# Kernel tuning notes

Hardware: AMD Instinct MI355X
Metric: run time of the kernel (lower is better)

Reference implementation:

```python
import jax, jax.numpy as jnp
import numpy as np

B, S, H, I = 4, 2048, 2048, 8192
LN_EPS = 1e-6  # DeepSpeed inference layer-norm epsilon


def setup_inputs() -> dict:
    key = jax.random.key(0)
    ks = jax.random.split(key, 10)
    return {
        "input": jax.random.normal(ks[0], (B, S, H), dtype=jnp.float32),
        "residual": jax.random.normal(ks[1], (B, S, H), dtype=jnp.float32),
        "residual_norm": jax.random.normal(ks[2], (B, S, H), dtype=jnp.float32),
        "bias": jax.random.normal(ks[3], (H,), dtype=jnp.float32) * 0.02,
        "gamma": jnp.ones((H,), dtype=jnp.float32) + jax.random.normal(ks[4], (H,), dtype=jnp.float32) * 0.02,
        "beta": jax.random.normal(ks[5], (H,), dtype=jnp.float32) * 0.02,
        "inter_w": jax.random.normal(ks[6], (H, I), dtype=jnp.float32) * 0.02,
        "inter_b": jax.random.normal(ks[7], (I,), dtype=jnp.float32) * 0.02,
        "output_w": jax.random.normal(ks[8], (I, H), dtype=jnp.float32) * 0.02,
        "output_b": jax.random.normal(ks[9], (H,), dtype=jnp.float32) * 0.02,
    }


def reference(input, residual, residual_norm, bias, gamma, beta,
              inter_w, inter_b, output_w, output_b):
    # --- mlp_gemm_func (pre-LN path, attn_nw is not None) ---
    # Fused: residual_add = attention_output + attention_bias + residual
    residual_add = input + residual + bias                    # [B,S,H]
    # LayerNorm over hidden dim
    mu = jnp.mean(residual_add, axis=-1, keepdims=True)
    var = jnp.mean(jnp.square(residual_add - mu), axis=-1, keepdims=True)
    ln = (residual_add - mu) * jax.lax.rsqrt(var + LN_EPS) * gamma + beta
    # GEMM + bias + GeLU, then second GEMM
    h = jax.nn.gelu(jnp.einsum("bsh,hi->bsi", ln, inter_w) + inter_b,
                    approximate=False)                        # [B,S,I]
    out = jnp.einsum("bsi,ih->bsh", h, output_w)              # [B,S,H]
    # --- residual_add_func (pre-LN, mlp_after_attn): mlp_out + residual_add + final_bias ---
    return out + residual_add + output_b
```

## Files before the change

kernel.cpp:

```cpp
#include <hip/hip_runtime.h>

typedef __attribute__((ext_vector_type(8))) __bf16 bf16x8;
typedef __attribute__((ext_vector_type(4))) float f32x4;

#define AS1(p) ((const __attribute__((address_space(1))) void*)(uintptr_t)(p))
#define AS3(p) ((__attribute__((address_space(3))) void*)(uint32_t)(uintptr_t)(p))
#define GLD16(gp, lp) __builtin_amdgcn_global_load_lds(AS1(gp), AS3(lp), 16, 0, 0)

static constexpr int Bb = 4, Ss = 2048, Hh = 2048, Ih = 8192;
static constexpr int Mm = Bb * Ss;

__device__ __forceinline__ float gelu_exact(float x) {
    return 0.5f * x * (1.0f + erff(x * 0.70710678118654752440f));
}

__global__ __launch_bounds__(256) void transpose_cvt(const float* __restrict__ src,
                                                     __bf16* __restrict__ dst,
                                                     int R, int C) {
    __shared__ float tile[32][33];
    const int tx = threadIdx.x, ty = threadIdx.y;
    const int cB = blockIdx.x * 32, rB = blockIdx.y * 32;
#pragma unroll
    for (int i = 0; i < 4; ++i)
        tile[ty + i * 8][tx] = src[(size_t)(rB + ty + i * 8) * C + cB + tx];
    __syncthreads();
#pragma unroll
    for (int i = 0; i < 4; ++i)
        dst[(size_t)(cB + ty + i * 8) * R + rB + tx] = (__bf16)tile[tx][ty + i * 8];
}

__global__ __launch_bounds__(256) void fused_ln(const float* __restrict__ input,
                                                const float* __restrict__ residual,
                                                const float* __restrict__ bias,
                                                const float* __restrict__ gamma,
                                                const float* __restrict__ beta,
                                                __bf16* __restrict__ lnb,
                                                __bf16* __restrict__ rab) {
    const int row = blockIdx.x;
    const int tid = threadIdx.x;
    const size_t base = (size_t)row * Hh;
    const int e = tid * 8;

    float4 x0 = *(const float4*)(input + base + e);
    float4 x1 = *(const float4*)(input + base + e + 4);
    float4 r0 = *(const float4*)(residual + base + e);
    float4 r1 = *(const float4*)(residual + base + e + 4);
    float4 b0 = *(const float4*)(bias + e);
    float4 b1 = *(const float4*)(bias + e + 4);

    float s[8];
    s[0] = x0.x + r0.x + b0.x; s[1] = x0.y + r0.y + b0.y;
    s[2] = x0.z + r0.z + b0.z; s[3] = x0.w + r0.w + b0.w;
    s[4] = x1.x + r1.x + b1.x; s[5] = x1.y + r1.y + b1.y;
    s[6] = x1.z + r1.z + b1.z; s[7] = x1.w + r1.w + b1.w;

    float sum = 0.f, sq = 0.f;
#pragma unroll
    for (int j = 0; j < 8; ++j) { sum += s[j]; sq += s[j] * s[j]; }
#pragma unroll
    for (int o = 32; o > 0; o >>= 1) {
        sum += __shfl_xor(sum, o);
        sq  += __shfl_xor(sq, o);
    }
    __shared__ float red[8];
    const int wv = tid >> 6, ln_ = tid & 63;
    if (ln_ == 0) { red[wv] = sum; red[4 + wv] = sq; }
    __syncthreads();
    sum = red[0] + red[1] + red[2] + red[3];
    sq  = red[4] + red[5] + red[6] + red[7];

    const float mu   = sum * (1.0f / Hh);
    const float var  = sq * (1.0f / Hh) - mu * mu;
    const float rstd = rsqrtf(var + 1e-6f);

    float4 g0 = *(const float4*)(gamma + e);
    float4 g1 = *(const float4*)(gamma + e + 4);
    float4 t0 = *(const float4*)(beta + e);
    float4 t1 = *(const float4*)(beta + e + 4);
    float g[8] = {g0.x, g0.y, g0.z, g0.w, g1.x, g1.y, g1.z, g1.w};
    float t[8] = {t0.x, t0.y, t0.z, t0.w, t1.x, t1.y, t1.z, t1.w};

    bf16x8 lv, rv;
#pragma unroll
    for (int j = 0; j < 8; ++j) {
        rv[j] = (__bf16)s[j];
        lv[j] = (__bf16)((s[j] - mu) * rstd * g[j] + t[j]);
    }
    *(bf16x8*)(lnb + base + e) = lv;
    *(bf16x8*)(rab + base + e) = rv;
}

#define CFENCE asm volatile("" ::: "memory")
#define BARX   do { CFENCE; __builtin_amdgcn_s_barrier(); CFENCE; } while (0)
#define SP1 __builtin_amdgcn_s_setprio(1)
#define SP0 __builtin_amdgcn_s_setprio(0)
#define VM2 asm volatile("s_waitcnt vmcnt(2)" ::: "memory")
#define VM0 asm volatile("s_waitcnt vmcnt(0)" ::: "memory")

__device__ __forceinline__ void rdA(bf16x8 (&af)[4][2], const char* p0, const char* p1,
                                    const int off) {
#pragma unroll
    for (int m = 0; m < 4; ++m) {
        af[m][0] = *(const bf16x8*)(p0 + off + m * 2048);
        af[m][1] = *(const bf16x8*)(p1 + off + m * 2048);
    }
}
__device__ __forceinline__ void rdB(bf16x8 (&bf)[2][2], const char* p0, const char* p1,
                                    const int off) {
#pragma unroll
    for (int n = 0; n < 2; ++n) {
        bf[n][0] = *(const bf16x8*)(p0 + off + n * 2048);
        bf[n][1] = *(const bf16x8*)(p1 + off + n * 2048);
    }
}
template <int MH, int NH>
__device__ __forceinline__ void mfmaQ(const bf16x8 (&a)[4][2], const bf16x8 (&b)[2][2],
                                      f32x4 (&acc)[8][4]) {
#pragma unroll
    for (int ks = 0; ks < 2; ++ks)
#pragma unroll
        for (int m = 0; m < 4; ++m)
#pragma unroll
            for (int n = 0; n < 2; ++n)
                acc[MH * 4 + m][NH * 2 + n] = __builtin_amdgcn_mfma_f32_16x16x32_bf16(
                    a[m][ks], b[n][ks], acc[MH * 4 + m][NH * 2 + n], 0, 0, 0);
}
__device__ __forceinline__ void stage2(const __bf16* src, __bf16* dst, const size_t row64) {
    GLD16(src, dst);
    GLD16(src + row64, dst + 4096);
}

#define GEMM_SETUP(Aptr, Btptr)                                                          \
    const int tid = threadIdx.x;                                                         \
    const int nbx = N >> 8;                                                              \
    const int nwg = gridDim.x;                                                           \
    const int cpx = nwg >> 3;                                                            \
    const int bid = blockIdx.x;                                                          \
    const int swz = (bid & 7) * cpx + (bid >> 3);                                        \
    const int by = swz / nbx, bx = swz - by * nbx;                                       \
    const int mBase = by << 8, nBase = bx << 8;                                          \
    const int wave = tid >> 6, lane = tid & 63;                                          \
    const int wr = wave >> 2, wc = wave & 3;                                             \
    const int NT = K >> 6;                                                               \
    const int NI = NT >> 1;                                                              \
    char* ldsc = (char*)lds;                                                             \
    const int laneCol0 = (((lane >> 4) << 4)) ^ ((lane & 7) << 4);                       \
    const int laneCol1 = laneCol0 ^ 64;                                                  \
    const int aLaneR = (lane & 15) << 7;                                                 \
    const int bLaneR = (((wc & 1) << 6) + (lane & 15)) << 7;                             \
    const char* pA[2][2] = {                                                             \
        {ldsc + (0 * 4 + wr) * 16384 + aLaneR + laneCol0,                                \
         ldsc + (0 * 4 + wr) * 16384 + aLaneR + laneCol1},                               \
        {ldsc + (1 * 4 + wr) * 16384 + aLaneR + laneCol0,                                \
         ldsc + (1 * 4 + wr) * 16384 + aLaneR + laneCol1}};                              \
    const char* pB[2][2] = {                                                             \
        {ldsc + (0 * 4 + 2 + (wc >> 1)) * 16384 + bLaneR + laneCol0,                     \
         ldsc + (0 * 4 + 2 + (wc >> 1)) * 16384 + bLaneR + laneCol1},                    \
        {ldsc + (1 * 4 + 2 + (wc >> 1)) * 16384 + bLaneR + laneCol0,                     \
         ldsc + (1 * 4 + 2 + (wc >> 1)) * 16384 + bLaneR + laneCol1}};                   \
    const int srow = tid >> 3;                                                           \
    const int scol = ((tid & 7) ^ (srow & 7)) << 3;                                      \
    const __bf16* aSt = (Aptr) + (size_t)(mBase + srow) * K + scol;                      \
    const __bf16* bSt = (Btptr) + (size_t)(nBase + srow) * K + scol;                     \
    __bf16* lw = lds + tid * 8;                                                          \
    const size_t row64 = (size_t)64 * K;                                                 \
    const size_t row128 = (size_t)128 * K;

#define STA(buf, h, t) stage2(aSt + (h) * row128 + (size_t)(t) * 64, lw + ((buf) * 4 + (h)) * 8192, row64)
#define STB(buf, h, t) stage2(bSt + (h) * row128 + (size_t)(t) * 64, lw + ((buf) * 4 + 2 + (h)) * 8192, row64)

__global__ __launch_bounds__(512, 2) void gemmX(const __bf16* __restrict__ A,
                                                const __bf16* __restrict__ Bt,
                                                const float* __restrict__ bias,
                                                __bf16* __restrict__ outH,
                                                int M, int N, int K) {
    __shared__ __align__(128) __bf16 lds[2 * 4 * 128 * 64];
    GEMM_SETUP(A, Bt)

    f32x4 acc[8][4] = {};
    bf16x8 af[4][2], b0[2][2], b1[2][2];

    STA(0, 0, 0); STA(0, 1, 0); STB(0, 0, 0); STB(0, 1, 0);
    STA(1, 0, 1); STA(1, 1, 1); STB(1, 0, 1); STB(1, 1, 1);
    VM0;
    BARX;
    rdA(af, pA[0][0], pA[0][1], 0);
    rdB(b0, pB[0][0], pB[0][1], 0);

#define TILEX(P, NP, BLO, BHI, PF, T2)                          \
    SP1; mfmaQ<0, 0>(af, BLO, acc); SP0;                        \
    rdB(BHI, pB[P][0], pB[P][1], 4096);                         \
    BARX;                                                       \
    SP1; mfmaQ<0, 1>(af, BHI, acc); SP0;                        \
    rdA(af, pA[P][0], pA[P][1], 8192);                          \
    VM0;                                                        \
    BARX;                                                       \
    SP1; mfmaQ<1, 1>(af, BHI, acc); SP0;                        \
    rdB(BHI, pB[NP][0], pB[NP][1], 0);                          \
    BARX;                                                       \
    SP1; mfmaQ<1, 0>(af, BLO, acc); SP0;                        \
    rdA(af, pA[NP][0], pA[NP][1], 0);                           \
    if (PF) { STA(P, 0, T2); STA(P, 1, T2); STB(P, 0, T2); STB(P, 1, T2); } \
    BARX;

    for (int i = 0; i < NI; ++i) {
        const int t0 = 2 * i, t1 = 2 * i + 1;
        const bool pf0 = (t0 + 2 < NT);
        const bool pf1 = (t1 + 2 < NT);
        TILEX(0, 1, b0, b1, pf0, t0 + 2)
        TILEX(1, 0, b1, b0, pf1, t1 + 2)
    }
#undef TILEX

    const int r0 = mBase + wr * 128 + ((lane >> 4) << 2);
    const int c0 = nBase + wc * 64 + (lane & 15);
    float bb[4];
#pragma unroll
    for (int nf = 0; nf < 4; ++nf) bb[nf] = bias[c0 + nf * 16];
#pragma unroll
    for (int mf = 0; mf < 8; ++mf) {
        const int row = r0 + mf * 16;
#pragma unroll
        for (int nf = 0; nf < 4; ++nf) {
            const int col = c0 + nf * 16;
#pragma unroll
            for (int j = 0; j < 4; ++j) {
                const size_t idx = (size_t)(row + j) * N + col;
                outH[idx] = (__bf16)gelu_exact(acc[mf][nf][j] + bb[nf]);
            }
        }
    }
}

__global__ __launch_bounds__(512, 2) void gemm256(const __bf16* __restrict__ A,
                                                  const __bf16* __restrict__ Bt,
                                                  const float* __restrict__ bias,
                                                  const __bf16* __restrict__ rab,
                                                  float* __restrict__ outF,
                                                  int M, int N, int K) {
    __shared__ __align__(128) __bf16 lds[2 * 4 * 128 * 64];
    GEMM_SETUP(A, Bt)

    f32x4 acc[8][4] = {};
    bf16x8 af[4][2], b0[2][2], b1[2][2];

    STA(0, 0, 0); STA(0, 1, 0); STB(0, 0, 0); STB(0, 1, 0);
    VM0;
    BARX;
    STB(1, 0, 1); STB(1, 1, 1);
    rdA(af, pA[0][0], pA[0][1], 0);
    rdB(b0, pB[0][0], pB[0][1], 0);

    for (int i = 0; i < NI; ++i) {
        const int t0 = 2 * i, t1 = 2 * i + 1;
        const bool pf0 = (t0 + 2 < NT);
        const bool pf1 = (t1 + 2 < NT);
        const bool last = (i == NI - 1);

        SP1; mfmaQ<0, 0>(af, b0, acc); SP0;
        rdB(b1, pB[0][0], pB[0][1], 4096);
        STA(1, 0, t1);
        BARX;
        SP1; mfmaQ<0, 1>(af, b1, acc); SP0;
        rdA(af, pA[0][0], pA[0][1], 8192);
        STA(1, 1, t1);
        BARX;
        SP1; mfmaQ<1, 1>(af, b1, acc); SP0;
        if (pf0) { STB(0, 0, t0 + 2); VM2; } else { VM0; }
        BARX;
        SP1; mfmaQ<1, 0>(af, b0, acc); SP0;
        rdA(af, pA[1][0], pA[1][1], 0);
        rdB(b0, pB[1][0], pB[1][1], 0);
        if (pf0) STB(0, 1, t0 + 2);
        BARX;
        SP1; mfmaQ<0, 0>(af, b0, acc); SP0;
        rdB(b1, pB[1][0], pB[1][1], 4096);
        if (pf0) STA(0, 0, t0 + 2);
        BARX;
        SP1; mfmaQ<0, 1>(af, b1, acc); SP0;
        rdA(af, pA[1][0], pA[1][1], 8192);
        if (pf0) STA(0, 1, t0 + 2);
        BARX;
        SP1; mfmaQ<1, 1>(af, b1, acc); SP0;
        if (pf1) { STB(1, 0, t1 + 2); VM2; } else { VM0; }
        BARX;
        SP1; mfmaQ<1, 0>(af, b0, acc); SP0;
        if (!last) {
            rdA(af, pA[0][0], pA[0][1], 0);
            rdB(b0, pB[0][0], pB[0][1], 0);
        }
        if (pf1) STB(1, 1, t1 + 2);
        BARX;
    }

    const int r0 = mBase + wr * 128 + ((lane >> 4) << 2);
    const int c0 = nBase + wc * 64 + (lane & 15);
    float bb[4];
#pragma unroll
    for (int nf = 0; nf < 4; ++nf) bb[nf] = bias[c0 + nf * 16];
#pragma unroll
    for (int mf = 0; mf < 8; ++mf) {
        const int row = r0 + mf * 16;
#pragma unroll
        for (int nf = 0; nf < 4; ++nf) {
            const int col = c0 + nf * 16;
#pragma unroll
            for (int j = 0; j < 4; ++j) {
                const size_t idx = (size_t)(row + j) * N + col;
                outF[idx] = acc[mf][nf][j] + bb[nf] + (float)rab[idx];
            }
        }
    }
}

extern "C" void kernel_launch(void* const* d_in, const int* in_sizes, int n_in,
                              void* d_out, int out_size, void* d_ws, size_t ws_size,
                              hipStream_t stream) {
    const float* input    = (const float*)d_in[0];
    const float* residual = (const float*)d_in[1];
    const float* bias     = (const float*)d_in[3];
    const float* gamma    = (const float*)d_in[4];
    const float* beta     = (const float*)d_in[5];
    const float* inter_w  = (const float*)d_in[6];
    const float* inter_b  = (const float*)d_in[7];
    const float* output_w = (const float*)d_in[8];
    const float* output_b = (const float*)d_in[9];
    float* out = (float*)d_out;

    __bf16* w1t  = (__bf16*)d_ws;
    __bf16* w2t  = w1t + (size_t)Ih * Hh;
    __bf16* lnb  = w2t + (size_t)Hh * Ih;
    __bf16* rab  = lnb + (size_t)Mm * Hh;
    __bf16* hbuf = rab + (size_t)Mm * Hh;

    transpose_cvt<<<dim3(Ih / 32, Hh / 32), dim3(32, 8), 0, stream>>>(inter_w, w1t, Hh, Ih);
    transpose_cvt<<<dim3(Hh / 32, Ih / 32), dim3(32, 8), 0, stream>>>(output_w, w2t, Ih, Hh);

    fused_ln<<<Mm, 256, 0, stream>>>(input, residual, bias, gamma, beta, lnb, rab);

    gemmX<<<dim3((Mm / 256) * (Ih / 256)), 512, 0, stream>>>(
        lnb, w1t, inter_b, hbuf, Mm, Ih, Hh);

    gemm256<<<dim3((Mm / 256) * (Hh / 256)), 512, 0, stream>>>(
        hbuf, w2t, output_b, rab, out, Mm, Hh, Ih);
}
```

Before: 599.8 us.

## Reschedule first GEMM main loop with staggered LDS staging and split MFMA/LDS reads

```diff
diff --git a/kernel.cpp b/kernel.cpp
--- a/kernel.cpp
+++ b/kernel.cpp
@@ -105,6 +105,15 @@
         af[m][1] = *(const bf16x8*)(p1 + off + m * 2048);
     }
 }
+template <int M0>
+__device__ __forceinline__ void rdA2(bf16x8 (&af)[4][2], const char* p0, const char* p1,
+                                     const int off) {
+#pragma unroll
+    for (int m = M0; m < M0 + 2; ++m) {
+        af[m][0] = *(const bf16x8*)(p0 + off + m * 2048);
+        af[m][1] = *(const bf16x8*)(p1 + off + m * 2048);
+    }
+}
 __device__ __forceinline__ void rdB(bf16x8 (&bf)[2][2], const char* p0, const char* p1,
                                     const int off) {
 #pragma unroll
@@ -120,6 +129,18 @@
     for (int ks = 0; ks < 2; ++ks)
 #pragma unroll
         for (int m = 0; m < 4; ++m)
+#pragma unroll
+            for (int n = 0; n < 2; ++n)
+                acc[MH * 4 + m][NH * 2 + n] = __builtin_amdgcn_mfma_f32_16x16x32_bf16(
+                    a[m][ks], b[n][ks], acc[MH * 4 + m][NH * 2 + n], 0, 0, 0);
+}
+template <int MH, int NH, int M0>
+__device__ __forceinline__ void mfmaP(const bf16x8 (&a)[4][2], const bf16x8 (&b)[2][2],
+                                      f32x4 (&acc)[8][4]) {
+#pragma unroll
+    for (int ks = 0; ks < 2; ++ks)
+#pragma unroll
+        for (int m = M0; m < M0 + 2; ++m)
 #pragma unroll
             for (int n = 0; n < 2; ++n)
                 acc[MH * 4 + m][NH * 2 + n] = __builtin_amdgcn_mfma_f32_16x16x32_bf16(
@@ -169,7 +190,7 @@
 #define STA(buf, h, t) stage2(aSt + (h) * row128 + (size_t)(t) * 64, lw + ((buf) * 4 + (h)) * 8192, row64)
 #define STB(buf, h, t) stage2(bSt + (h) * row128 + (size_t)(t) * 64, lw + ((buf) * 4 + 2 + (h)) * 8192, row64)
 
-__global__ __launch_bounds__(512, 2) void gemmX(const __bf16* __restrict__ A,
+__global__ __launch_bounds__(512, 2) void gemmS(const __bf16* __restrict__ A,
                                                 const __bf16* __restrict__ Bt,
                                                 const float* __restrict__ bias,
                                                 __bf16* __restrict__ outH,
@@ -181,36 +202,58 @@
     bf16x8 af[4][2], b0[2][2], b1[2][2];
 
     STA(0, 0, 0); STA(0, 1, 0); STB(0, 0, 0); STB(0, 1, 0);
-    STA(1, 0, 1); STA(1, 1, 1); STB(1, 0, 1); STB(1, 1, 1);
     VM0;
     BARX;
+    STB(1, 0, 1); STB(1, 1, 1);
     rdA(af, pA[0][0], pA[0][1], 0);
     rdB(b0, pB[0][0], pB[0][1], 0);
-
-#define TILEX(P, NP, BLO, BHI, PF, T2)                          \
-    SP1; mfmaQ<0, 0>(af, BLO, acc); SP0;                        \
-    rdB(BHI, pB[P][0], pB[P][1], 4096);                         \
-    BARX;                                                       \
-    SP1; mfmaQ<0, 1>(af, BHI, acc); SP0;                        \
-    rdA(af, pA[P][0], pA[P][1], 8192);                          \
-    VM0;                                                        \
-    BARX;                                                       \
-    SP1; mfmaQ<1, 1>(af, BHI, acc); SP0;                        \
-    rdB(BHI, pB[NP][0], pB[NP][1], 0);                          \
-    BARX;                                                       \
-    SP1; mfmaQ<1, 0>(af, BLO, acc); SP0;                        \
-    rdA(af, pA[NP][0], pA[NP][1], 0);                           \
-    if (PF) { STA(P, 0, T2); STA(P, 1, T2); STB(P, 0, T2); STB(P, 1, T2); } \
-    BARX;
 
     for (int i = 0; i < NI; ++i) {
         const int t0 = 2 * i, t1 = 2 * i + 1;
         const bool pf0 = (t0 + 2 < NT);
         const bool pf1 = (t1 + 2 < NT);
-        TILEX(0, 1, b0, b1, pf0, t0 + 2)
-        TILEX(1, 0, b1, b0, pf1, t1 + 2)
-    }
-#undef TILEX
+
+        rdB(b1, pB[0][0], pB[0][1], 4096);
+        SP1; mfmaQ<0, 0>(af, b0, acc); SP0;
+        STA(1, 0, t1);
+        BARX;
+        SP1; mfmaP<0, 1, 0>(af, b1, acc);
+        rdA2<0>(af, pA[0][0], pA[0][1], 8192);
+        mfmaP<0, 1, 2>(af, b1, acc); SP0;
+        rdA2<2>(af, pA[0][0], pA[0][1], 8192);
+        STA(1, 1, t1);
+        BARX;
+        SP1; mfmaQ<1, 1>(af, b1, acc); SP0;
+        if (pf0) { STB(0, 0, t0 + 2); VM2; } else { VM0; }
+        BARX;
+        SP1; mfmaP<1, 0, 0>(af, b0, acc);
+        rdA2<0>(af, pA[1][0], pA[1][1], 0);
+        mfmaP<1, 0, 2>(af, b0, acc); SP0;
+        rdA2<2>(af, pA[1][0], pA[1][1], 0);
+        rdB(b0, pB[1][0], pB[1][1], 0);
+        if (pf0) STB(0, 1, t0 + 2);
+        BARX;
+        rdB(b1, pB[1][0], pB[1][1], 4096);
+        SP1; mfmaQ<0, 0>(af, b0, acc); SP0;
+        if (pf0) STA(0, 0, t0 + 2);
+        BARX;
+        SP1; mfmaP<0, 1, 0>(af, b1, acc);
+        rdA2<0>(af, pA[1][0], pA[1][1], 8192);
+        mfmaP<0, 1, 2>(af, b1, acc); SP0;
+        rdA2<2>(af, pA[1][0], pA[1][1], 8192);
+        if (pf0) STA(0, 1, t0 + 2);
+        BARX;
+        SP1; mfmaQ<1, 1>(af, b1, acc); SP0;
+        if (pf1) { STB(1, 0, t1 + 2); VM2; } else { VM0; }
+        BARX;
+        SP1; mfmaP<1, 0, 0>(af, b0, acc);
+        rdA2<0>(af, pA[0][0], pA[0][1], 0);
+        mfmaP<1, 0, 2>(af, b0, acc); SP0;
+        rdA2<2>(af, pA[0][0], pA[0][1], 0);
+        rdB(b0, pB[0][0], pB[0][1], 0);
+        if (pf1) STB(1, 1, t1 + 2);
+        BARX;
+    }
 
     const int r0 = mBase + wr * 128 + ((lane >> 4) << 2);
     const int c0 = nBase + wc * 64 + (lane & 15);
@@ -338,7 +381,7 @@
 
     fused_ln<<<Mm, 256, 0, stream>>>(input, residual, bias, gamma, beta, lnb, rab);
 
-    gemmX<<<dim3((Mm / 256) * (Ih / 256)), 512, 0, stream>>>(
+    gemmS<<<dim3((Mm / 256) * (Ih / 256)), 512, 0, stream>>>(
         lnb, w1t, inter_b, hbuf, Mm, Ih, Hh);
 
     gemm256<<<dim3((Mm / 256) * (Hh / 256)), 512, 0, stream>>>(
```

Result: no change. 590.3 us (-1.6%).
